# Kernel tuning notes

Measured on AMD Instinct MI355X. Metric: run time of the kernel, lower is better.

## Reference

```python
import jax, jax.numpy as jnp
import numpy as np

B, S, E, H = 2, 2048, 2048, 16
D = E // H  # head_dim = 128
EPS = 1e-5


def setup_inputs() -> dict:
    key = jax.random.key(0)
    ks = jax.random.split(key, 16)
    s_e = 1.0 / np.sqrt(E)
    s_f = 1.0 / np.sqrt(4 * E)
    return {
        "x": jax.random.normal(ks[0], (B, S, E), jnp.float32),
        "ln1_w": jnp.ones((E,), jnp.float32) + 0.01 * jax.random.normal(ks[1], (E,)),
        "ln1_b": 0.01 * jax.random.normal(ks[2], (E,)),
        "wq": s_e * jax.random.normal(ks[3], (E, E), jnp.float32),
        "wk": s_e * jax.random.normal(ks[4], (E, E), jnp.float32),
        "wv": s_e * jax.random.normal(ks[5], (E, E), jnp.float32),
        "wo": s_e * jax.random.normal(ks[6], (E, E), jnp.float32),
        "bo": 0.01 * jax.random.normal(ks[7], (E,)),
        "ln2_w": jnp.ones((E,), jnp.float32) + 0.01 * jax.random.normal(ks[8], (E,)),
        "ln2_b": 0.01 * jax.random.normal(ks[9], (E,)),
        "w1": s_e * jax.random.normal(ks[10], (E, 4 * E), jnp.float32),
        "b1": 0.01 * jax.random.normal(ks[11], (4 * E,)),
        "w2": s_f * jax.random.normal(ks[12], (4 * E, E), jnp.float32),
        "b2": 0.01 * jax.random.normal(ks[13], (E,)),
    }


def _layernorm(x, w, b):
    mu = jnp.mean(x, axis=-1, keepdims=True)
    var = jnp.var(x, axis=-1, keepdims=True)
    return (x - mu) * jax.lax.rsqrt(var + EPS) * w + b


def _attention(x, wq, wk, wv, wo, bo):
    # x: [B,S,E] -> q,k,v: [B,H,S,D]
    def split(t):
        return t.reshape(B, S, H, D).transpose(0, 2, 1, 3)
    q = split(x @ wq)
    k = split(x @ wk)
    v = split(x @ wv)
    scores = jnp.einsum("bhqd,bhkd->bhqk", q, k)  # [B,H,S,S]
    causal = jnp.triu(jnp.ones((S, S), bool), k=1)
    scores = jnp.where(causal, -jnp.inf, scores)
    # NOTE: faithful to source -- scaling applied after masking, inside softmax arg
    attn = jax.nn.softmax(scores / np.sqrt(D), axis=-1)
    ctx = jnp.einsum("bhqk,bhkd->bhqd", attn, v)
    ctx = ctx.transpose(0, 2, 1, 3).reshape(B, S, E)
    return ctx @ wo + bo


def reference(x, ln1_w, ln1_b, wq, wk, wv, wo, bo, ln2_w, ln2_b, w1, b1, w2, b2):
    shortcut = x
    x1 = _layernorm(x, ln1_w, ln1_b)
    attn_out = _attention(x1, wq, wk, wv, wo, bo)
    a = attn_out + shortcut
    # NOTE: faithful to source quirk -- second shortcut is post-LN1 x1, not a
    y = _layernorm(a, ln2_w, ln2_b)
    y = jax.nn.gelu(y @ w1 + b1, approximate=False) @ w2 + b2
    return x1 + y
```

## Files before the change

kernel.cpp:

```cpp
#include <hip/hip_runtime.h>
#include <math.h>

typedef unsigned short u16;
typedef unsigned int u32;
typedef __attribute__((ext_vector_type(8))) short short8;
typedef __attribute__((ext_vector_type(4))) float f32x4;
typedef __attribute__((ext_vector_type(16))) float f32x16;
typedef __attribute__((ext_vector_type(4))) u32 u32x4;
typedef __attribute__((ext_vector_type(2))) u32 u32x2;

#define DEVFN static __device__ __forceinline__

DEVFN u16 f2bf(float x) {
  union { float f; u32 u; } v; v.f = x;
  u32 r = v.u + 0x7fffu + ((v.u >> 16) & 1u);
  return (u16)(r >> 16);
}
DEVFN float bf2f(u16 h) {
  union { u32 u; float f; } v; v.u = ((u32)h) << 16;
  return v.f;
}
DEVFN u32 packbf2(float a, float b) {
  return (u32)f2bf(a) | ((u32)f2bf(b) << 16);
}
DEVFN void gl2lds16(const u16* g, u16* l) {
  __builtin_amdgcn_global_load_lds(
      (const __attribute__((address_space(1))) u32*)g,
      (__attribute__((address_space(3))) u32*)l, 16, 0, 0);
}
DEVFN float gelu_exact(float v) {
  float s = v * 0.70710678118654752f;
  float ax = fabsf(s);
  float t = __builtin_amdgcn_rcpf(1.0f + 0.3275911f * ax);
  float poly = t * (0.254829592f +
               t * (-0.284496736f +
               t * (1.421413741f +
               t * (-1.453152027f + t * 1.061405429f))));
  float e = __expf(-s * s);
  float er = 1.0f - poly * e;
  er = (s < 0.f) ? -er : er;
  return 0.5f * v * (1.0f + er);
}

#define VMW0() asm volatile("s_waitcnt vmcnt(0)" ::: "memory")
#define CFENCE() asm volatile("" ::: "memory")
#define BARRIER() do { CFENCE(); __builtin_amdgcn_s_barrier(); CFENCE(); } while (0)

__global__ __launch_bounds__(256) void tconvall_k(
    const float* __restrict__ wq, const float* __restrict__ wk,
    const float* __restrict__ wv, const float* __restrict__ wo,
    const float* __restrict__ w1, const float* __restrict__ w2,
    u16* __restrict__ wqt, u16* __restrict__ wkt, u16* __restrict__ wvt,
    u16* __restrict__ wot, u16* __restrict__ w1t, u16* __restrict__ w2t) {
  __shared__ float tile[32][33];
  int b = blockIdx.x;
  const float* in; u16* out; int K, N, tn, tk;
  if (b < 16384) {
    int wsel = b >> 12;
    int loc = b & 4095;
    in = (wsel == 0) ? wq : (wsel == 1) ? wk : (wsel == 2) ? wv : wo;
    out = (wsel == 0) ? wqt : (wsel == 1) ? wkt : (wsel == 2) ? wvt : wot;
    K = 2048; N = 2048; tn = loc & 63; tk = loc >> 6;
  } else if (b < 32768) {
    int loc = b - 16384; in = w1; out = w1t; K = 2048; N = 8192;
    tn = loc & 255; tk = loc >> 8;
  } else {
    int loc = b - 32768; in = w2; out = w2t; K = 8192; N = 2048;
    tn = loc & 63; tk = loc >> 6;
  }
  int n0 = tn << 5, k0 = tk << 5;
  int tx = threadIdx.x & 31, ty = threadIdx.x >> 5;
#pragma unroll
  for (int i = 0; i < 32; i += 8)
    tile[ty + i][tx] = in[(long)(k0 + ty + i) * N + n0 + tx];
  __syncthreads();
#pragma unroll
  for (int i = 0; i < 32; i += 8)
    out[(long)(n0 + ty + i) * K + k0 + tx] = f2bf(tile[tx][ty + i]);
}

__global__ __launch_bounds__(256) void ln1_k(const float* __restrict__ x,
                                             const float* __restrict__ w,
                                             const float* __restrict__ b,
                                             float* __restrict__ y32,
                                             u16* __restrict__ y16) {
  long base = (long)blockIdx.x * 2048;
  int t = threadIdx.x;
  float4 v0 = ((const float4*)(x + base))[2 * t];
  float4 v1 = ((const float4*)(x + base))[2 * t + 1];
  float xv[8];
  *(float4*)xv = v0; *(float4*)(xv + 4) = v1;
  float s = 0.f, ss = 0.f;
#pragma unroll
  for (int i = 0; i < 8; ++i) { s += xv[i]; ss += xv[i] * xv[i]; }
#pragma unroll
  for (int m = 1; m < 64; m <<= 1) { s += __shfl_xor(s, m); ss += __shfl_xor(ss, m); }
  __shared__ float rs[4], rss[4];
  int wave = t >> 6;
  if ((t & 63) == 0) { rs[wave] = s; rss[wave] = ss; }
  __syncthreads();
  s = rs[0] + rs[1] + rs[2] + rs[3];
  ss = rss[0] + rss[1] + rss[2] + rss[3];
  float mean = s * (1.f / 2048.f);
  float var = ss * (1.f / 2048.f) - mean * mean;
  float inv = rsqrtf(var + 1e-5f);
  float wv[8], bv[8];
  *(float4*)wv = ((const float4*)w)[2 * t]; *(float4*)(wv + 4) = ((const float4*)w)[2 * t + 1];
  *(float4*)bv = ((const float4*)b)[2 * t]; *(float4*)(bv + 4) = ((const float4*)b)[2 * t + 1];
  float yv[8];
#pragma unroll
  for (int i = 0; i < 8; ++i) yv[i] = (xv[i] - mean) * inv * wv[i] + bv[i];
  ((float4*)(y32 + base))[2 * t] = *(float4*)yv;
  ((float4*)(y32 + base))[2 * t + 1] = *(float4*)(yv + 4);
  u32x4 ov;
#pragma unroll
  for (int i = 0; i < 4; ++i) ov[i] = packbf2(yv[2 * i], yv[2 * i + 1]);
  ((u32x4*)(y16 + base))[t] = ov;
}

__global__ __launch_bounds__(256) void ln2_k(const u16* __restrict__ a,
                                             const float* __restrict__ w,
                                             const float* __restrict__ b,
                                             u16* __restrict__ y) {
  long base = (long)blockIdx.x * 2048;
  int t = threadIdx.x;
  u32x4 pv = ((const u32x4*)(a + base))[t];
  float xv[8];
#pragma unroll
  for (int i = 0; i < 4; ++i) {
    xv[2 * i] = bf2f((u16)(pv[i] & 0xffffu));
    xv[2 * i + 1] = bf2f((u16)(pv[i] >> 16));
  }
  float s = 0.f, ss = 0.f;
#pragma unroll
  for (int i = 0; i < 8; ++i) { s += xv[i]; ss += xv[i] * xv[i]; }
#pragma unroll
  for (int m = 1; m < 64; m <<= 1) { s += __shfl_xor(s, m); ss += __shfl_xor(ss, m); }
  __shared__ float rs[4], rss[4];
  int wave = t >> 6;
  if ((t & 63) == 0) { rs[wave] = s; rss[wave] = ss; }
  __syncthreads();
  s = rs[0] + rs[1] + rs[2] + rs[3];
  ss = rss[0] + rss[1] + rss[2] + rss[3];
  float mean = s * (1.f / 2048.f);
  float var = ss * (1.f / 2048.f) - mean * mean;
  float inv = rsqrtf(var + 1e-5f);
  float wv[8], bv[8];
  *(float4*)wv = ((const float4*)w)[2 * t]; *(float4*)(wv + 4) = ((const float4*)w)[2 * t + 1];
  *(float4*)bv = ((const float4*)b)[2 * t]; *(float4*)(bv + 4) = ((const float4*)b)[2 * t + 1];
  u32x4 ov;
#pragma unroll
  for (int i = 0; i < 4; ++i) {
    float y0 = (xv[2 * i] - mean) * inv * wv[2 * i] + bv[2 * i];
    float y1 = (xv[2 * i + 1] - mean) * inv * wv[2 * i + 1] + bv[2 * i + 1];
    ov[i] = packbf2(y0, y1);
  }
  ((u32x4*)(y + base))[t] = ov;
}

template <int MODE>
__global__ __launch_bounds__(256, 2) void gemm9_k(const u16* __restrict__ A,
                                                  const u16* __restrict__ W,
                                                  void* __restrict__ outp,
                                                  const float* __restrict__ bias,
                                                  const float* __restrict__ resid,
                                                  int M, int N, int K) {
  __shared__ __align__(16) u16 lds[2][16384];
  const int t = threadIdx.x, lane = t & 63, wave = t >> 6;
  const int l31 = lane & 31, hi = lane >> 5;
  const int wm = wave >> 1, wn = wave & 1;
  const int nM = M >> 7;
  const int nwg = gridDim.x * gridDim.y;
  const int orig = blockIdx.y * gridDim.x + blockIdx.x;
  const int sw = (orig & 7) * (nwg >> 3) + (orig >> 3);
  const long m0 = (long)(sw % nM) * 128, n0 = (long)(sw / nM) * 128;
  const int nt = K >> 6;
  const long Kl = K;
  const int srow = lane >> 3, schk = lane & 7;

  auto stA = [&](int b, int ts) {
#pragma unroll
    for (int q = 0; q < 4; ++q) {
      int rb = q * 32 + wave * 8;
      int rr = rb + srow;
      gl2lds16(A + (m0 + rr) * Kl + (long)ts * 64 + (schk ^ (rr & 7)) * 8,
               &lds[b][rb * 64]);
    }
  };
  auto stB = [&](int b, int ts) {
#pragma unroll
    for (int q = 0; q < 4; ++q) {
      int rb = q * 32 + wave * 8;
      int rr = rb + srow;
      gl2lds16(W + (n0 + rr) * Kl + (long)ts * 64 + (schk ^ (rr & 7)) * 8,
               &lds[b][8192 + rb * 64]);
    }
  };

  f32x16 acc[2][2] = {};

  stA(0, 0); stB(0, 0);

  for (int tt = 0; tt < nt; ++tt) {
    const int cur = tt & 1;
    const int ts = (tt + 1 < nt) ? tt + 1 : tt;
    VMW0();
    BARRIER();
    stA(cur ^ 1, ts); stB(cur ^ 1, ts);
    const u16* Lc = &lds[cur][0];
    short8 af[2][4], bf[2][4];
#pragma unroll
    for (int i = 0; i < 2; ++i) {
      int row = wm * 64 + i * 32 + l31;
#pragma unroll
      for (int s = 0; s < 4; ++s)
        af[i][s] = *(const short8*)(Lc + row * 64 + (((s << 1) | hi) ^ (row & 7)) * 8);
    }
#pragma unroll
    for (int j = 0; j < 2; ++j) {
      int row = wn * 64 + j * 32 + l31;
#pragma unroll
      for (int s = 0; s < 4; ++s)
        bf[j][s] = *(const short8*)(Lc + 8192 + row * 64 + (((s << 1) | hi) ^ (row & 7)) * 8);
    }
    __builtin_amdgcn_s_setprio(1);
#pragma unroll
    for (int i = 0; i < 2; ++i)
#pragma unroll
      for (int j = 0; j < 2; ++j)
#pragma unroll
        for (int s = 0; s < 4; ++s)
          acc[i][j] = __builtin_amdgcn_mfma_f32_32x32x16_bf16(
              af[i][s], bf[j][s], acc[i][j], 0, 0, 0);
    __builtin_amdgcn_s_setprio(0);
  }
  VMW0();

  const long Nl = N;
#pragma unroll
  for (int i = 0; i < 2; ++i) {
#pragma unroll
    for (int j = 0; j < 2; ++j) {
#pragma unroll
      for (int r = 0; r < 16; ++r) {
        long mg = m0 + wm * 64 + i * 32 + (r & 3) + 8 * (r >> 2) + 4 * hi;
        long ng = n0 + wn * 64 + j * 32 + l31;
        float v = acc[i][j][r];
        if constexpr (MODE == 0) {
          long which = ng >> 11;
          long nloc = ng & 2047;
          long bb = mg >> 11, sq = mg & 2047;
          long hh = nloc >> 7, dd = nloc & 127;
          long idx = (which < 2) ? (((bb * 16 + hh) * 2048 + sq) * 128 + dd)
                                 : (((bb * 16 + hh) * 128 + dd) * 2048 + sq);
          ((u16*)outp)[which * 8388608 + idx] = f2bf(v);
        } else if constexpr (MODE == 2) {
          v += bias[ng] + resid[mg * Nl + ng];
          ((u16*)outp)[mg * Nl + ng] = f2bf(v);
        } else if constexpr (MODE == 3) {
          v = gelu_exact(v + bias[ng]);
          ((u16*)outp)[mg * Nl + ng] = f2bf(v);
        } else {
          v += bias[ng] + resid[mg * Nl + ng];
          ((float*)outp)[mg * Nl + ng] = v;
        }
      }
    }
  }
}

__global__ __launch_bounds__(256, 2) void attn2_k(const u16* __restrict__ Qp,
                                                  const u16* __restrict__ Kp,
                                                  const u16* __restrict__ Vp,
                                                  u16* __restrict__ ctx) {
  __shared__ __align__(16) u16 KsL[2][64 * 128];
  __shared__ __align__(16) u16 VsL[2][128 * 64];
  const int qt = gridDim.x - 1 - blockIdx.x;
  const int bh = blockIdx.y;
  const int t = threadIdx.x, lane = t & 63, wave = t >> 6;
  const int l31 = lane & 31, hi = lane >> 5;
  const int q0 = qt * 128, qw0 = q0 + wave * 32;
  const int qg = qw0 + l31;
  const u16* Qh = Qp + (long)bh * 2048 * 128;
  const u16* Kh = Kp + (long)bh * 2048 * 128;
  const u16* Vh = Vp + (long)bh * 128 * 2048;
  const int nkt = qt * 2 + 2;
  const int ktmax = (qw0 + 31) >> 6;
  const float cs = 0.12753042923810058f;

  short8 qf[8];
#pragma unroll
  for (int ds = 0; ds < 8; ++ds)
    qf[ds] = *(const short8*)(Qh + (long)qg * 128 + ds * 16 + hi * 8);

  f32x16 O0 = {}, O1 = {}, O2 = {}, O3 = {};
  float m = -INFINITY, l = 0.f;

  auto stage = [&](int b, int kt) {
#pragma unroll
    for (int q = 0; q < 4; ++q) {
      int r = wave * 16 + q * 4 + (lane >> 4);
      int c = (lane & 15) ^ (r & 15);
      gl2lds16(Kh + ((long)kt * 64 + r) * 128 + c * 8,
               &KsL[b][(wave * 16 + q * 4) * 128]);
    }
#pragma unroll
    for (int q = 0; q < 4; ++q) {
      int r = wave * 32 + q * 8 + (lane >> 3);
      int c = (lane & 7) ^ (r & 7);
      gl2lds16(Vh + (long)r * 2048 + kt * 64 + c * 8,
               &VsL[b][(wave * 32 + q * 8) * 64]);
    }
  };

  stage(0, 0);
  VMW0(); BARRIER();

  for (int kt = 0; kt < nkt; ++kt) {
    const int cur = kt & 1;
    if (kt + 1 < nkt) stage(cur ^ 1, kt + 1);
    if (kt <= ktmax) {
      f32x16 S0 = {}, S1 = {};
      __builtin_amdgcn_s_setprio(1);
#pragma unroll
      for (int ds = 0; ds < 8; ++ds) {
        int c0 = ((ds * 2 + hi) ^ (l31 & 15)) * 8;
        short8 k0 = *(const short8*)(&KsL[cur][l31 * 128 + c0]);
        int r1 = 32 + l31;
        int c1 = ((ds * 2 + hi) ^ (r1 & 15)) * 8;
        short8 k1 = *(const short8*)(&KsL[cur][r1 * 128 + c1]);
        S0 = __builtin_amdgcn_mfma_f32_32x32x16_bf16(k0, qf[ds], S0, 0, 0, 0);
        S1 = __builtin_amdgcn_mfma_f32_32x32x16_bf16(k1, qf[ds], S1, 0, 0, 0);
      }
      __builtin_amdgcn_s_setprio(0);
      float p[32];
#pragma unroll
      for (int i = 0; i < 16; ++i) { p[i] = S0[i]; p[16 + i] = S1[i]; }
      if (kt * 64 + 63 > qw0) {
#pragma unroll
        for (int ks = 0; ks < 2; ++ks)
#pragma unroll
          for (int r = 0; r < 16; ++r) {
            int kg = kt * 64 + ks * 32 + (r & 3) + 8 * (r >> 2) + 4 * hi;
            if (kg > qg) p[ks * 16 + r] = -INFINITY;
          }
      }
      float tmax = p[0];
#pragma unroll
      for (int i = 1; i < 32; ++i) tmax = fmaxf(tmax, p[i]);
      tmax = fmaxf(tmax, __shfl_xor(tmax, 32));
      float mnew = fmaxf(m, tmax);
      float corr = __builtin_amdgcn_exp2f((m - mnew) * cs);
      float ls = 0.f;
#pragma unroll
      for (int i = 0; i < 32; ++i) {
        p[i] = __builtin_amdgcn_exp2f((p[i] - mnew) * cs);
        ls += p[i];
      }
      ls += __shfl_xor(ls, 32);
      l = l * corr + ls;
      m = mnew;
#pragma unroll
      for (int i = 0; i < 16; ++i) {
        O0[i] *= corr; O1[i] *= corr; O2[i] *= corr; O3[i] *= corr;
      }
      short8 pf[4];
#pragma unroll
      for (int gg = 0; gg < 4; ++gg) {
        u32 u_, v_, w_, z_;
        asm("v_cvt_pk_bf16_f32 %0, %1, %2" : "=v"(u_) : "v"(p[gg * 8 + 0]), "v"(p[gg * 8 + 1]));
        asm("v_cvt_pk_bf16_f32 %0, %1, %2" : "=v"(v_) : "v"(p[gg * 8 + 2]), "v"(p[gg * 8 + 3]));
        asm("v_cvt_pk_bf16_f32 %0, %1, %2" : "=v"(w_) : "v"(p[gg * 8 + 4]), "v"(p[gg * 8 + 5]));
        asm("v_cvt_pk_bf16_f32 %0, %1, %2" : "=v"(z_) : "v"(p[gg * 8 + 6]), "v"(p[gg * 8 + 7]));
        asm("v_permlane32_swap_b32 %0, %1" : "+v"(u_), "+v"(w_));
        asm("v_permlane32_swap_b32 %0, %1" : "+v"(v_), "+v"(z_));
        union { u32 w4[4]; short8 s; } cv;
        cv.w4[0] = u_; cv.w4[1] = v_; cv.w4[2] = w_; cv.w4[3] = z_;
        pf[gg] = cv.s;
      }
      __builtin_amdgcn_s_setprio(1);
#define PVROW(ds, OO)                                                          \
  {                                                                            \
    int row = (ds)*32 + l31;                                                   \
    _Pragma("unroll") for (int gg = 0; gg < 4; ++gg) {                         \
      short8 vf = *(const short8*)(&VsL[cur][row * 64 +                        \
                                             (((gg * 2 + hi) ^ (row & 7)) * 8)]); \
      OO = __builtin_amdgcn_mfma_f32_32x32x16_bf16(vf, pf[gg], OO, 0, 0, 0);   \
    }                                                                          \
  }
      PVROW(0, O0); PVROW(1, O1); PVROW(2, O2); PVROW(3, O3);
#undef PVROW
      __builtin_amdgcn_s_setprio(0);
    }
    VMW0(); BARRIER();
  }

  const float inv = 1.f / l;
  u16* cp = ctx + ((long)(bh >> 4) * 2048 + qg) * 2048 + (bh & 15) * 128;
#define WROUT(OO, dsb)                                                         \
  _Pragma("unroll") for (int rg = 0; rg < 4; ++rg) {                           \
    int d = (dsb)*32 + 8 * rg + 4 * hi;                                        \
    u32x2 wv;                                                                  \
    wv[0] = packbf2(OO[4 * rg] * inv, OO[4 * rg + 1] * inv);                   \
    wv[1] = packbf2(OO[4 * rg + 2] * inv, OO[4 * rg + 3] * inv);               \
    *(u32x2*)(cp + d) = wv;                                                    \
  }
  WROUT(O0, 0); WROUT(O1, 1); WROUT(O2, 2); WROUT(O3, 3);
#undef WROUT
}

extern "C" void kernel_launch(void* const* d_in, const int* in_sizes, int n_in,
                              void* d_out, int out_size, void* d_ws, size_t ws_size,
                              hipStream_t stream) {
  const float* x = (const float*)d_in[0];
  const float* ln1w = (const float*)d_in[1];
  const float* ln1b = (const float*)d_in[2];
  const float* wq = (const float*)d_in[3];
  const float* wk = (const float*)d_in[4];
  const float* wv = (const float*)d_in[5];
  const float* wo = (const float*)d_in[6];
  const float* bo = (const float*)d_in[7];
  const float* ln2w = (const float*)d_in[8];
  const float* ln2b = (const float*)d_in[9];
  const float* w1 = (const float*)d_in[10];
  const float* b1 = (const float*)d_in[11];
  const float* w2 = (const float*)d_in[12];
  const float* b2 = (const float*)d_in[13];
  float* out = (float*)d_out;
  char* ws = (char*)d_ws;

  float* x1f = (float*)(ws + 0);
  u16* x1b = (u16*)(ws + 33554432);
  u16* wqt = (u16*)(ws + 50331648);
  u16* wkt = (u16*)(ws + 58720256);
  u16* wvt = (u16*)(ws + 67108864);
  u16* wot = (u16*)(ws + 75497472);
  u16* w1t = (u16*)(ws + 83886080);
  u16* w2t = (u16*)(ws + 117440512);
  u16* qb = (u16*)(ws + 150994944);
  u16* kb = (u16*)(ws + 167772160);
  u16* vb = (u16*)(ws + 184549376);
  u16* ctxb = (u16*)(ws + 201326592);
  u16* ab = (u16*)(ws + 218103808);
  u16* y0b = (u16*)(ws + 234881024);
  u16* hb = qb;

  tconvall_k<<<49152, 256, 0, stream>>>(wq, wk, wv, wo, w1, w2,
                                        wqt, wkt, wvt, wot, w1t, w2t);
  ln1_k<<<4096, 256, 0, stream>>>(x, ln1w, ln1b, x1f, x1b);
  gemm9_k<0><<<dim3(32, 48), 256, 0, stream>>>(x1b, wqt, qb, nullptr, nullptr, 4096, 6144, 2048);
  attn2_k<<<dim3(16, 32), 256, 0, stream>>>(qb, kb, vb, ctxb);
  gemm9_k<2><<<dim3(32, 16), 256, 0, stream>>>(ctxb, wot, ab, bo, x, 4096, 2048, 2048);
  ln2_k<<<4096, 256, 0, stream>>>(ab, ln2w, ln2b, y0b);
  gemm9_k<3><<<dim3(32, 64), 256, 0, stream>>>(y0b, w1t, hb, b1, nullptr, 4096, 8192, 2048);
  gemm9_k<4><<<dim3(32, 16), 256, 0, stream>>>(hb, w2t, out, b2, x1f, 4096, 2048, 8192);
}
```

Baseline: 745.2 us.

## Rework GEMM to 128x256 tiles with 8 waves, 16x16 MFMA and deeper prefetch

Replaces the 256-thread 128x128 GEMM with a 512-thread kernel computing 128x256 output tiles over K-steps of 32, using 16x16x32 bf16 MFMA and a new LDS swizzle. Loads are issued two stages ahead into a double buffer, with partial vmcnt waits so global-to-LDS copies overlap compute. The larger N tile is meant to raise arithmetic intensity and reuse of A, and the extra waves to improve latency hiding. The cost is more barriers per K-step, halved grid sizes and a different occupancy target (launch_bounds 512,4).

```diff
diff --git a/kernel.cpp b/kernel.cpp
--- a/kernel.cpp
+++ b/kernel.cpp
@@ -42,7 +42,9 @@
   return 0.5f * v * (1.0f + er);
 }
 
+#define VMW3() asm volatile("s_waitcnt vmcnt(3)" ::: "memory")
 #define VMW0() asm volatile("s_waitcnt vmcnt(0)" ::: "memory")
+#define LGKM0() asm volatile("s_waitcnt lgkmcnt(0)" ::: "memory")
 #define CFENCE() asm volatile("" ::: "memory")
 #define BARRIER() do { CFENCE(); __builtin_amdgcn_s_barrier(); CFENCE(); } while (0)
 
@@ -159,92 +161,88 @@
 }
 
 template <int MODE>
-__global__ __launch_bounds__(256, 2) void gemm9_k(const u16* __restrict__ A,
+__global__ __launch_bounds__(512, 4) void gemmA_k(const u16* __restrict__ A,
                                                   const u16* __restrict__ W,
                                                   void* __restrict__ outp,
                                                   const float* __restrict__ bias,
                                                   const float* __restrict__ resid,
                                                   int M, int N, int K) {
-  __shared__ __align__(16) u16 lds[2][16384];
+  __shared__ __align__(16) u16 lds[2][12288];
   const int t = threadIdx.x, lane = t & 63, wave = t >> 6;
-  const int l31 = lane & 31, hi = lane >> 5;
-  const int wm = wave >> 1, wn = wave & 1;
+  const int g = lane >> 4, r16 = lane & 15;
+  const int wm = wave >> 2, wn = wave & 3;
   const int nM = M >> 7;
   const int nwg = gridDim.x * gridDim.y;
   const int orig = blockIdx.y * gridDim.x + blockIdx.x;
-  const int sw = (orig & 7) * (nwg >> 3) + (orig >> 3);
-  const long m0 = (long)(sw % nM) * 128, n0 = (long)(sw / nM) * 128;
-  const int nt = K >> 6;
+  const int sw = (nwg & 7) ? orig : ((orig & 7) * (nwg >> 3) + (orig >> 3));
+  const long m0 = (long)(sw % nM) * 128, n0 = (long)(sw / nM) * 256;
+  const int nt = K >> 5;
   const long Kl = K;
-  const int srow = lane >> 3, schk = lane & 7;
-
-  auto stA = [&](int b, int ts) {
-#pragma unroll
-    for (int q = 0; q < 4; ++q) {
-      int rb = q * 32 + wave * 8;
-      int rr = rb + srow;
-      gl2lds16(A + (m0 + rr) * Kl + (long)ts * 64 + (schk ^ (rr & 7)) * 8,
-               &lds[b][rb * 64]);
+  const int lr = lane >> 2, lc = lane & 3;
+
+  auto stage = [&](int b, int ts) {
+    {
+      int row = wave * 16 + lr;
+      int c = lc ^ (row & 3) ^ ((row >> 2) & 3);
+      gl2lds16(A + (m0 + row) * Kl + (long)ts * 32 + c * 8,
+               &lds[b][wave * 512]);
+    }
+#pragma unroll
+    for (int j = 0; j < 2; ++j) {
+      int row = j * 128 + wave * 16 + lr;
+      int c = lc ^ (row & 3) ^ ((row >> 2) & 3);
+      gl2lds16(W + (n0 + row) * Kl + (long)ts * 32 + c * 8,
+               &lds[b][4096 + j * 4096 + wave * 512]);
     }
   };
-  auto stB = [&](int b, int ts) {
-#pragma unroll
-    for (int q = 0; q < 4; ++q) {
-      int rb = q * 32 + wave * 8;
-      int rr = rb + srow;
-      gl2lds16(W + (n0 + rr) * Kl + (long)ts * 64 + (schk ^ (rr & 7)) * 8,
-               &lds[b][8192 + rb * 64]);
-    }
-  };
-
-  f32x16 acc[2][2] = {};
-
-  stA(0, 0); stB(0, 0);
+
+  f32x4 acc[4][4] = {};
+
+  stage(0, 0);
+  stage(1, 1);
+  VMW3();
+  BARRIER();
 
   for (int tt = 0; tt < nt; ++tt) {
     const int cur = tt & 1;
-    const int ts = (tt + 1 < nt) ? tt + 1 : tt;
-    VMW0();
+    const int ts = (tt + 2 < nt) ? tt + 2 : nt - 1;
+    const u16* Lc = &lds[cur][0];
+    short8 af[4], bf[4];
+#pragma unroll
+    for (int i = 0; i < 4; ++i) {
+      int row = wm * 64 + i * 16 + r16;
+      int c = g ^ (row & 3) ^ ((row >> 2) & 3);
+      af[i] = *(const short8*)(Lc + row * 32 + c * 8);
+    }
+#pragma unroll
+    for (int j = 0; j < 4; ++j) {
+      int row = wn * 64 + j * 16 + r16;
+      int c = g ^ (row & 3) ^ ((row >> 2) & 3);
+      bf[j] = *(const short8*)(Lc + 4096 + row * 32 + c * 8);
+    }
+    LGKM0();
     BARRIER();
-    stA(cur ^ 1, ts); stB(cur ^ 1, ts);
-    const u16* Lc = &lds[cur][0];
-    short8 af[2][4], bf[2][4];
-#pragma unroll
-    for (int i = 0; i < 2; ++i) {
-      int row = wm * 64 + i * 32 + l31;
-#pragma unroll
-      for (int s = 0; s < 4; ++s)
-        af[i][s] = *(const short8*)(Lc + row * 64 + (((s << 1) | hi) ^ (row & 7)) * 8);
-    }
-#pragma unroll
-    for (int j = 0; j < 2; ++j) {
-      int row = wn * 64 + j * 32 + l31;
-#pragma unroll
-      for (int s = 0; s < 4; ++s)
-        bf[j][s] = *(const short8*)(Lc + 8192 + row * 64 + (((s << 1) | hi) ^ (row & 7)) * 8);
-    }
+    stage(cur, ts);
     __builtin_amdgcn_s_setprio(1);
 #pragma unroll
-    for (int i = 0; i < 2; ++i)
-#pragma unroll
-      for (int j = 0; j < 2; ++j)
-#pragma unroll
-        for (int s = 0; s < 4; ++s)
-          acc[i][j] = __builtin_amdgcn_mfma_f32_32x32x16_bf16(
-              af[i][s], bf[j][s], acc[i][j], 0, 0, 0);
+    for (int i = 0; i < 4; ++i)
+#pragma unroll
+      for (int j = 0; j < 4; ++j)
+        acc[i][j] = __builtin_amdgcn_mfma_f32_16x16x32_bf16(af[i], bf[j], acc[i][j], 0, 0, 0);
     __builtin_amdgcn_s_setprio(0);
-  }
-  VMW0();
+    VMW3();
+    BARRIER();
+  }
 
   const long Nl = N;
 #pragma unroll
-  for (int i = 0; i < 2; ++i) {
-#pragma unroll
-    for (int j = 0; j < 2; ++j) {
-#pragma unroll
-      for (int r = 0; r < 16; ++r) {
-        long mg = m0 + wm * 64 + i * 32 + (r & 3) + 8 * (r >> 2) + 4 * hi;
-        long ng = n0 + wn * 64 + j * 32 + l31;
+  for (int i = 0; i < 4; ++i) {
+#pragma unroll
+    for (int j = 0; j < 4; ++j) {
+#pragma unroll
+      for (int r = 0; r < 4; ++r) {
+        long mg = m0 + wm * 64 + i * 16 + g * 4 + r;
+        long ng = n0 + wn * 64 + j * 16 + r16;
         float v = acc[i][j][r];
         if constexpr (MODE == 0) {
           long which = ng >> 11;
@@ -448,10 +446,10 @@
   tconvall_k<<<49152, 256, 0, stream>>>(wq, wk, wv, wo, w1, w2,
                                         wqt, wkt, wvt, wot, w1t, w2t);
   ln1_k<<<4096, 256, 0, stream>>>(x, ln1w, ln1b, x1f, x1b);
-  gemm9_k<0><<<dim3(32, 48), 256, 0, stream>>>(x1b, wqt, qb, nullptr, nullptr, 4096, 6144, 2048);
+  gemmA_k<0><<<dim3(32, 24), 512, 0, stream>>>(x1b, wqt, qb, nullptr, nullptr, 4096, 6144, 2048);
   attn2_k<<<dim3(16, 32), 256, 0, stream>>>(qb, kb, vb, ctxb);
-  gemm9_k<2><<<dim3(32, 16), 256, 0, stream>>>(ctxb, wot, ab, bo, x, 4096, 2048, 2048);
+  gemmA_k<2><<<dim3(32, 8), 512, 0, stream>>>(ctxb, wot, ab, bo, x, 4096, 2048, 2048);
   ln2_k<<<4096, 256, 0, stream>>>(ab, ln2w, ln2b, y0b);
-  gemm9_k<3><<<dim3(32, 64), 256, 0, stream>>>(y0b, w1t, hb, b1, nullptr, 4096, 8192, 2048);
-  gemm9_k<4><<<dim3(32, 16), 256, 0, stream>>>(hb, w2t, out, b2, x1f, 4096, 2048, 8192);
-}
+  gemmA_k<3><<<dim3(32, 32), 512, 0, stream>>>(y0b, w1t, hb, b1, nullptr, 4096, 8192, 2048);
+  gemmA_k<4><<<dim3(32, 8), 512, 0, stream>>>(hb, w2t, out, b2, x1f, 4096, 2048, 8192);
+}
```

New measurement: 723.8 us. -2.9%, faster.
